# Kernel tuning notes

Hardware: AMD Instinct MI355X
Metric: run time of the kernel (lower is better)

The kernel has to match this reference:

```python
import jax, jax.numpy as jnp
import numpy as np

N = 100000
E = 1250000
D = 64
R = 16


def _glorot(key, shape):
    fan_in, fan_out = shape[-2], shape[-1]
    lim = jnp.sqrt(6.0 / (fan_in + fan_out))
    return jax.random.uniform(key, shape, jnp.float32, -lim, lim)


def setup_inputs() -> dict:
    key = jax.random.key(0)
    ks = jax.random.split(key, 9)
    x = jax.random.normal(ks[0], (N, D), jnp.float32)
    edge_index = jax.random.randint(ks[1], (2, E), 0, N, jnp.int64 if jax.config.jax_enable_x64 else jnp.int32).astype(jnp.int32)
    edge_type = jax.random.randint(ks[2], (E,), 0, R).astype(jnp.int32)
    return {
        "x": x,
        "edge_index": edge_index,
        "edge_type": edge_type,
        "W1": _glorot(ks[3], (R, D, D)),
        "sw1": _glorot(ks[4], (D, D)),
        "b1": jnp.zeros((D,), jnp.float32),
        "W2": _glorot(ks[5], (R, D, D)),
        "sw2": _glorot(ks[6], (D, D)),
        "b2": jnp.zeros((D,), jnp.float32),
    }


def _rgcn_layer(x, src, dst, edge_type, W, sw, b, residual):
    # self transform [N, O]
    out = x @ sw
    # per-relation transform of all nodes: [N, R, O] (avoids [E, D, O] gathered weights,
    # same math as bmm(x_j, W[edge_type]))
    xW = jnp.einsum('nd,rdo->nro', x, W)
    msg = xW[src, edge_type]                      # [E, O] per-edge messages
    agg = jax.ops.segment_sum(msg, dst, num_segments=N)  # scatter-add aggregate
    out = out + agg
    if residual:
        out = out + x  # Identity residual (in == out channels)
    out = out + b
    return jax.nn.relu(out)


def reference(x, edge_index, edge_type, W1, sw1, b1, W2, sw2, b2):
    src, dst = edge_index[0], edge_index[1]
    # layer 1: residual=True; layer 2: encoding=False -> no residual.
    # activation (relu) applied after every layer by RGCN.forward; dropout p=0 / eval -> no-op.
    h = _rgcn_layer(x, src, dst, edge_type, W1, sw1, b1, residual=True)
    h = _rgcn_layer(h, src, dst, edge_type, W2, sw2, b2, residual=False)
    return h
```

## Files before the change

### kernel.cpp

```cpp
#include <hip/hip_runtime.h>
#include <hip/hip_bf16.h>

#define NN 100000
#define NE 1250000
#define DD 64
#define RR 16
#define NP 17
#define NTILE 6250

typedef __attribute__((ext_vector_type(8))) short s16x8;
typedef __attribute__((ext_vector_type(4))) float f32x4;

static __device__ __forceinline__ unsigned short f2bf(float v) {
    __hip_bfloat16 h = __float2bfloat16(v);
    return __builtin_bit_cast(unsigned short, h);
}
static __device__ __forceinline__ float bf2f(unsigned short u) {
    unsigned int w = ((unsigned int)u) << 16;
    return __builtin_bit_cast(float, w);
}
static __device__ __forceinline__ unsigned int pack2(float a, float b) {
    return ((unsigned int)f2bf(b) << 16) | (unsigned int)f2bf(a);
}


__global__ void hist_dst(const int* __restrict__ dst, int* __restrict__ cnt) {
    int e = blockIdx.x * 256 + threadIdx.x;
    if (e < NE) atomicAdd(&cnt[dst[e]], 1);
}

__global__ __launch_bounds__(256) void scan1(const int* __restrict__ cnt,
                                             int* __restrict__ rp, int* __restrict__ part) {
    __shared__ int s[256];
    int i = blockIdx.x * 256 + threadIdx.x;
    int v = (i < NN) ? cnt[i] : 0;
    s[threadIdx.x] = v;
    __syncthreads();
    for (int off = 1; off < 256; off <<= 1) {
        int t = (threadIdx.x >= off) ? s[threadIdx.x - off] : 0;
        __syncthreads();
        s[threadIdx.x] += t;
        __syncthreads();
    }
    if (i < NN) rp[i] = s[threadIdx.x] - v;
    if (threadIdx.x == 255) part[blockIdx.x] = s[255];
}

#define NBLK_SCAN 391
__global__ void scan2(int* __restrict__ part, int* __restrict__ rp) {
    __shared__ int s[NBLK_SCAN];
    if (threadIdx.x < NBLK_SCAN) s[threadIdx.x] = part[threadIdx.x];
    __syncthreads();
    if (threadIdx.x == 0) {
        int acc = 0;
        for (int b = 0; b < NBLK_SCAN; ++b) { int t = s[b]; s[b] = acc; acc += t; }
        rp[NN] = NE;
    }
    __syncthreads();
    if (threadIdx.x < NBLK_SCAN) part[threadIdx.x] = s[threadIdx.x];
}

__global__ void scan3(int* __restrict__ rp, const int* __restrict__ part, int* __restrict__ cur) {
    int i = blockIdx.x * 256 + threadIdx.x;
    if (i < NN) {
        int v = rp[i] + part[blockIdx.x];
        rp[i] = v;
        cur[i] = v;
    }
}

__global__ void scatter_dst(const int* __restrict__ src, const int* __restrict__ dst,
                            const int* __restrict__ et, int* __restrict__ cur,
                            int* __restrict__ sg) {
    int e = blockIdx.x * 256 + threadIdx.x;
    if (e >= NE) return;
    int p = atomicAdd(&cur[dst[e]], 1);
    sg[p] = et[e] * NN + src[e];
}


__global__ void prep_w2(const float* __restrict__ W1, const float* __restrict__ sw1,
                        const float* __restrict__ W2, const float* __restrict__ sw2,
                        unsigned short* __restrict__ wt) {
    int i = blockIdx.x * 256 + threadIdx.x;
    if (i >= 2 * NP * DD * DD) return;
    int d = i & 63;
    int o = (i >> 6) & 63;
    int p = (i >> 12) % NP;
    int l = i / (NP * DD * DD);
    const float* src;
    if (p < 16) src = (l ? W2 : W1) + p * DD * DD;
    else        src = (l ? sw2 : sw1);
    wt[i] = f2bf(src[d * DD + o]);
}

__global__ void prep_x2(const float* __restrict__ x, unsigned short* __restrict__ xb) {
    int i = blockIdx.x * blockDim.x + threadIdx.x;
    if (i < NN * DD) xb[i] = f2bf(x[i]);
}

__global__ __launch_bounds__(256) void xw_kernel(
    const unsigned short* __restrict__ xb,
    const unsigned short* __restrict__ wt,
    unsigned short* __restrict__ tab)
{
    const int wid  = threadIdx.x >> 6;
    const int lane = threadIdx.x & 63;
    const int c = lane & 15;
    const int q = lane >> 4;
    const int t = blockIdx.x * 4 + wid;
    if (t >= NTILE) return;
    const int n0 = t * 16;
    const int p0 = blockIdx.y * 4;
    const int p1 = min(p0 + 4, NP);

    const unsigned short* xrow = xb + (size_t)(n0 + c) * DD + q * 8;
    s16x8 b0 = *(const s16x8*)(xrow);
    s16x8 b1 = *(const s16x8*)(xrow + 32);

    for (int p = p0; p < p1; ++p) {
        const unsigned short* wp = wt + p * (DD * DD);
        uint2* orow = (uint2*)(tab + ((size_t)p * NN + n0 + c) * DD);
        #pragma unroll
        for (int nb = 0; nb < 4; ++nb) {
            const unsigned short* wrow = wp + (nb * 16 + c) * DD + q * 8;
            s16x8 a0 = *(const s16x8*)(wrow);
            s16x8 a1 = *(const s16x8*)(wrow + 32);
            f32x4 acc = {0.f, 0.f, 0.f, 0.f};
            acc = __builtin_amdgcn_mfma_f32_16x16x32_bf16(a0, b0, acc, 0, 0, 0);
            acc = __builtin_amdgcn_mfma_f32_16x16x32_bf16(a1, b1, acc, 0, 0, 0);
            uint2 pk;
            pk.x = pack2(acc[0], acc[1]);
            pk.y = pack2(acc[2], acc[3]);
            orow[nb * 4 + q] = pk;
        }
    }
}

__global__ __launch_bounds__(256) void agg_kernel(
    const unsigned short* __restrict__ tab,
    const int* __restrict__ rp,
    const int* __restrict__ sg,
    const float* __restrict__ bias,
    const float* __restrict__ xres,
    float* __restrict__ outf,
    unsigned short* __restrict__ outb)
{
    const int wid  = threadIdx.x >> 6;
    const int lane = threadIdx.x & 63;
    const int n = blockIdx.x * 4 + wid;
    const int h  = lane >> 5;
    const int ol = lane & 31;

    float a0 = 0.f, a1 = 0.f;
    int e = rp[n];
    const int e1 = rp[n + 1];
    for (; e + 4 <= e1; e += 4) {
        int r0 = sg[e + h];
        int r1 = sg[e + 2 + h];
        unsigned int u0 = *(const unsigned int*)(tab + (size_t)r0 * DD + ol * 2);
        unsigned int u1 = *(const unsigned int*)(tab + (size_t)r1 * DD + ol * 2);
        a0 += bf2f((unsigned short)u0) + bf2f((unsigned short)u1);
        a1 += bf2f((unsigned short)(u0 >> 16)) + bf2f((unsigned short)(u1 >> 16));
    }
    for (; e + 2 <= e1; e += 2) {
        int r0 = sg[e + h];
        unsigned int u0 = *(const unsigned int*)(tab + (size_t)r0 * DD + ol * 2);
        a0 += bf2f((unsigned short)u0);
        a1 += bf2f((unsigned short)(u0 >> 16));
    }
    if (e < e1 && h == 0) {
        int r0 = sg[e];
        unsigned int u0 = *(const unsigned int*)(tab + (size_t)r0 * DD + ol * 2);
        a0 += bf2f((unsigned short)u0);
        a1 += bf2f((unsigned short)(u0 >> 16));
    }
    a0 += __shfl_xor(a0, 32, 64);
    a1 += __shfl_xor(a1, 32, 64);

    {
        unsigned int u = *(const unsigned int*)(tab + ((size_t)16 * NN + n) * DD + ol * 2);
        a0 += bf2f((unsigned short)u);
        a1 += bf2f((unsigned short)(u >> 16));
    }
    const float2 bv = *(const float2*)(bias + ol * 2);
    a0 += bv.x; a1 += bv.y;
    if (xres) {
        const float2 rv = *(const float2*)(xres + (size_t)n * DD + ol * 2);
        a0 += rv.x; a1 += rv.y;
    }
    a0 = fmaxf(a0, 0.f);
    a1 = fmaxf(a1, 0.f);

    if (h == 0) {
        if (outb)
            *(unsigned int*)(outb + (size_t)n * DD + ol * 2) = pack2(a0, a1);
        if (outf) {
            float2 v = {a0, a1};
            *(float2*)(outf + (size_t)n * DD + ol * 2) = v;
        }
    }
}


extern "C" void kernel_launch(void* const* d_in, const int* in_sizes, int n_in,
                              void* d_out, int out_size, void* d_ws, size_t ws_size,
                              hipStream_t stream)
{
    (void)in_sizes; (void)n_in; (void)out_size; (void)ws_size;
    const float* x    = (const float*)d_in[0];
    const int*   ei   = (const int*)d_in[1];
    const int*   et   = (const int*)d_in[2];
    const float* W1   = (const float*)d_in[3];
    const float* sw1  = (const float*)d_in[4];
    const float* b1   = (const float*)d_in[5];
    const float* W2   = (const float*)d_in[6];
    const float* sw2  = (const float*)d_in[7];
    const float* b2   = (const float*)d_in[8];
    float* out = (float*)d_out;

    const int* src = ei;
    const int* dst = ei + NE;

    char* ws = (char*)d_ws;

    unsigned short* tab  = (unsigned short*)(ws);
    unsigned short* xb   = (unsigned short*)(ws + 217600000);
    unsigned short* h1b  = (unsigned short*)(ws + 230400000);
    unsigned short* wt2  = (unsigned short*)(ws + 243200000);
    int* sg   = (int*)(ws + 243478528);
    int* rp   = (int*)(ws + 248478528);
    int* cur  = (int*)(ws + 248878544);
    int* cnt  = (int*)(ws + 249278544);
    int* part = (int*)(ws + 249678544);

    const int NB_E    = (NE + 255) / 256;
    const int NB_ELEM = (NN * DD + 255) / 256;

    hipMemsetAsync(cnt, 0, NN * sizeof(int), stream);
    hist_dst<<<NB_E, 256, 0, stream>>>(dst, cnt);
    scan1<<<NBLK_SCAN, 256, 0, stream>>>(cnt, rp, part);
    scan2<<<1, 512, 0, stream>>>(part, rp);
    scan3<<<NBLK_SCAN, 256, 0, stream>>>(rp, part, cur);
    scatter_dst<<<NB_E, 256, 0, stream>>>(src, dst, et, cur, sg);

    prep_w2<<<(2 * NP * DD * DD + 255) / 256, 256, 0, stream>>>(W1, sw1, W2, sw2, wt2);
    prep_x2<<<NB_ELEM, 256, 0, stream>>>(x, xb);

    const int NB_XW  = (NTILE + 3) / 4;
    const int NB_AGG = NN / 4;

    xw_kernel<<<dim3(NB_XW, 5), 256, 0, stream>>>(xb, wt2, tab);
    agg_kernel<<<NB_AGG, 256, 0, stream>>>(tab, rp, sg, b1, x, nullptr, h1b);

    xw_kernel<<<dim3(NB_XW, 5), 256, 0, stream>>>(h1b, wt2 + NP * DD * DD, tab);
    agg_kernel<<<NB_AGG, 256, 0, stream>>>(tab, rp, sg, b2, nullptr, out, nullptr);
}
```

Baseline: 598.2 us.

## Stage xW tile stores through LDS and give each agg node a half-wave

The xW kernel now writes each 16x64 bf16 output tile into padded LDS first, then copies it to global memory with contiguous coalesced 8-byte stores instead of scattered row-fragment stores. The aggregation kernel now gives each node a 32-lane half-wave instead of a full wave split into two halves. Each lane gathers four edges per iteration with no cross-half shuffle reduction, and the self term, bias and residual are loaded up front. This aims to raise store coalescing and memory-level parallelism in the gather, at the cost of extra LDS traffic and a more divergent edge tail.

New measurement: 535.5 us. -10.5%, faster.

```diff
diff --git a/kernel.cpp b/kernel.cpp
--- a/kernel.cpp
+++ b/kernel.cpp
@@ -7,6 +7,8 @@
 #define RR 16
 #define NP 17
 #define NTILE 6250
+#define NBLK_SCAN 391
+#define LST 68
 
 typedef __attribute__((ext_vector_type(8))) short s16x8;
 typedef __attribute__((ext_vector_type(4))) float f32x4;
@@ -46,7 +48,6 @@
     if (threadIdx.x == 255) part[blockIdx.x] = s[255];
 }
 
-#define NBLK_SCAN 391
 __global__ void scan2(int* __restrict__ part, int* __restrict__ rp) {
     __shared__ int s[NBLK_SCAN];
     if (threadIdx.x < NBLK_SCAN) s[threadIdx.x] = part[threadIdx.x];
@@ -88,10 +89,10 @@
     int o = (i >> 6) & 63;
     int p = (i >> 12) % NP;
     int l = i / (NP * DD * DD);
-    const float* src;
-    if (p < 16) src = (l ? W2 : W1) + p * DD * DD;
-    else        src = (l ? sw2 : sw1);
-    wt[i] = f2bf(src[d * DD + o]);
+    const float* srcp;
+    if (p < 16) srcp = (l ? W2 : W1) + p * DD * DD;
+    else        srcp = (l ? sw2 : sw1);
+    wt[i] = f2bf(srcp[d * DD + o]);
 }
 
 __global__ void prep_x2(const float* __restrict__ x, unsigned short* __restrict__ xb) {
@@ -104,6 +105,7 @@
     const unsigned short* __restrict__ wt,
     unsigned short* __restrict__ tab)
 {
+    __shared__ unsigned short lds[4][16 * LST];
     const int wid  = threadIdx.x >> 6;
     const int lane = threadIdx.x & 63;
     const int c = lane & 15;
@@ -118,9 +120,10 @@
     s16x8 b0 = *(const s16x8*)(xrow);
     s16x8 b1 = *(const s16x8*)(xrow + 32);
 
+    unsigned short* lw = lds[wid];
+
     for (int p = p0; p < p1; ++p) {
         const unsigned short* wp = wt + p * (DD * DD);
-        uint2* orow = (uint2*)(tab + ((size_t)p * NN + n0 + c) * DD);
         #pragma unroll
         for (int nb = 0; nb < 4; ++nb) {
             const unsigned short* wrow = wp + (nb * 16 + c) * DD + q * 8;
@@ -132,7 +135,16 @@
             uint2 pk;
             pk.x = pack2(acc[0], acc[1]);
             pk.y = pack2(acc[2], acc[3]);
-            orow[nb * 4 + q] = pk;
+            *(uint2*)&lw[c * LST + nb * 16 + q * 4] = pk;
+        }
+        unsigned short* gbase = tab + ((size_t)p * NN + n0) * DD;
+        #pragma unroll
+        for (int j = 0; j < 4; ++j) {
+            int i8 = lane + 64 * j;
+            int node = i8 >> 4;
+            int k8 = i8 & 15;
+            uint2 v = *(const uint2*)&lw[node * LST + k8 * 4];
+            *(uint2*)(gbase + (size_t)i8 * 4) = v;
         }
     }
 }
@@ -143,62 +155,62 @@
     const int* __restrict__ sg,
     const float* __restrict__ bias,
     const float* __restrict__ xres,
-    float* __restrict__ outf,
-    unsigned short* __restrict__ outb)
+    unsigned short* __restrict__ outb,
+    float* __restrict__ outf)
 {
-    const int wid  = threadIdx.x >> 6;
-    const int lane = threadIdx.x & 63;
-    const int n = blockIdx.x * 4 + wid;
-    const int h  = lane >> 5;
-    const int ol = lane & 31;
-
-    float a0 = 0.f, a1 = 0.f;
+    const int hw = threadIdx.x >> 5;
+    const int ll = threadIdx.x & 31;
+    const int n = blockIdx.x * 8 + hw;
+    const unsigned int* t32 = (const unsigned int*)tab;
+
+    unsigned int us = t32[((size_t)16 * NN + n) * 32 + ll];
+    const float2 bv = *(const float2*)(bias + ll * 2);
+    float a0 = bv.x + bf2f((unsigned short)us);
+    float a1 = bv.y + bf2f((unsigned short)(us >> 16));
+    if (xres) {
+        const float2 rv = *(const float2*)(xres + (size_t)n * DD + ll * 2);
+        a0 += rv.x; a1 += rv.y;
+    }
+
     int e = rp[n];
     const int e1 = rp[n + 1];
     for (; e + 4 <= e1; e += 4) {
-        int r0 = sg[e + h];
-        int r1 = sg[e + 2 + h];
-        unsigned int u0 = *(const unsigned int*)(tab + (size_t)r0 * DD + ol * 2);
-        unsigned int u1 = *(const unsigned int*)(tab + (size_t)r1 * DD + ol * 2);
+        int r0 = sg[e], r1 = sg[e + 1], r2 = sg[e + 2], r3 = sg[e + 3];
+        unsigned int u0 = t32[(size_t)r0 * 32 + ll];
+        unsigned int u1 = t32[(size_t)r1 * 32 + ll];
+        unsigned int u2 = t32[(size_t)r2 * 32 + ll];
+        unsigned int u3 = t32[(size_t)r3 * 32 + ll];
         a0 += bf2f((unsigned short)u0) + bf2f((unsigned short)u1);
         a1 += bf2f((unsigned short)(u0 >> 16)) + bf2f((unsigned short)(u1 >> 16));
-    }
-    for (; e + 2 <= e1; e += 2) {
-        int r0 = sg[e + h];
-        unsigned int u0 = *(const unsigned int*)(tab + (size_t)r0 * DD + ol * 2);
-        a0 += bf2f((unsigned short)u0);
-        a1 += bf2f((unsigned short)(u0 >> 16));
-    }
-    if (e < e1 && h == 0) {
-        int r0 = sg[e];
-        unsigned int u0 = *(const unsigned int*)(tab + (size_t)r0 * DD + ol * 2);
-        a0 += bf2f((unsigned short)u0);
-        a1 += bf2f((unsigned short)(u0 >> 16));
-    }
-    a0 += __shfl_xor(a0, 32, 64);
-    a1 += __shfl_xor(a1, 32, 64);
-
+        a0 += bf2f((unsigned short)u2) + bf2f((unsigned short)u3);
+        a1 += bf2f((unsigned short)(u2 >> 16)) + bf2f((unsigned short)(u3 >> 16));
+    }
     {
-        unsigned int u = *(const unsigned int*)(tab + ((size_t)16 * NN + n) * DD + ol * 2);
-        a0 += bf2f((unsigned short)u);
-        a1 += bf2f((unsigned short)(u >> 16));
-    }
-    const float2 bv = *(const float2*)(bias + ol * 2);
-    a0 += bv.x; a1 += bv.y;
-    if (xres) {
-        const float2 rv = *(const float2*)(xres + (size_t)n * DD + ol * 2);
-        a0 += rv.x; a1 += rv.y;
-    }
+        const int m = e1 - e;
+        int rA = (m > 0) ? sg[e]     : -1;
+        int rB = (m > 1) ? sg[e + 1] : -1;
+        int rC = (m > 2) ? sg[e + 2] : -1;
+        if (rA >= 0) {
+            unsigned int u = t32[(size_t)rA * 32 + ll];
+            a0 += bf2f((unsigned short)u); a1 += bf2f((unsigned short)(u >> 16));
+        }
+        if (rB >= 0) {
+            unsigned int u = t32[(size_t)rB * 32 + ll];
+            a0 += bf2f((unsigned short)u); a1 += bf2f((unsigned short)(u >> 16));
+        }
+        if (rC >= 0) {
+            unsigned int u = t32[(size_t)rC * 32 + ll];
+            a0 += bf2f((unsigned short)u); a1 += bf2f((unsigned short)(u >> 16));
+        }
+    }
+
     a0 = fmaxf(a0, 0.f);
     a1 = fmaxf(a1, 0.f);
-
-    if (h == 0) {
-        if (outb)
-            *(unsigned int*)(outb + (size_t)n * DD + ol * 2) = pack2(a0, a1);
-        if (outf) {
-            float2 v = {a0, a1};
-            *(float2*)(outf + (size_t)n * DD + ol * 2) = v;
-        }
+    if (outb)
+        *(unsigned int*)(outb + (size_t)n * DD + ll * 2) = pack2(a0, a1);
+    if (outf) {
+        float2 v = {a0, a1};
+        *(float2*)(outf + (size_t)n * DD + ll * 2) = v;
     }
 }
 
@@ -219,11 +231,10 @@
     const float* b2   = (const float*)d_in[8];
     float* out = (float*)d_out;
 
-    const int* src = ei;
-    const int* dst = ei + NE;
+    const int* srcA = ei;
+    const int* dstA = ei + NE;
 
     char* ws = (char*)d_ws;
-
     unsigned short* tab  = (unsigned short*)(ws);
     unsigned short* xb   = (unsigned short*)(ws + 217600000);
     unsigned short* h1b  = (unsigned short*)(ws + 230400000);
@@ -238,21 +249,22 @@
     const int NB_ELEM = (NN * DD + 255) / 256;
 
     hipMemsetAsync(cnt, 0, NN * sizeof(int), stream);
-    hist_dst<<<NB_E, 256, 0, stream>>>(dst, cnt);
+    hist_dst<<<NB_E, 256, 0, stream>>>(dstA, cnt);
     scan1<<<NBLK_SCAN, 256, 0, stream>>>(cnt, rp, part);
     scan2<<<1, 512, 0, stream>>>(part, rp);
     scan3<<<NBLK_SCAN, 256, 0, stream>>>(rp, part, cur);
-    scatter_dst<<<NB_E, 256, 0, stream>>>(src, dst, et, cur, sg);
+    scatter_dst<<<NB_E, 256, 0, stream>>>(srcA, dstA, et, cur, sg);
 
     prep_w2<<<(2 * NP * DD * DD + 255) / 256, 256, 0, stream>>>(W1, sw1, W2, sw2, wt2);
     prep_x2<<<NB_ELEM, 256, 0, stream>>>(x, xb);
 
     const int NB_XW  = (NTILE + 3) / 4;
-    const int NB_AGG = NN / 4;
+    const int NB_AGG = NN / 8;
+    const int WPL = NP * DD * DD;
 
     xw_kernel<<<dim3(NB_XW, 5), 256, 0, stream>>>(xb, wt2, tab);
-    agg_kernel<<<NB_AGG, 256, 0, stream>>>(tab, rp, sg, b1, x, nullptr, h1b);
-
-    xw_kernel<<<dim3(NB_XW, 5), 256, 0, stream>>>(h1b, wt2 + NP * DD * DD, tab);
-    agg_kernel<<<NB_AGG, 256, 0, stream>>>(tab, rp, sg, b2, nullptr, out, nullptr);
-}
+    agg_kernel<<<NB_AGG, 256, 0, stream>>>(tab, rp, sg, b1, x, h1b, nullptr);
+
+    xw_kernel<<<dim3(NB_XW, 5), 256, 0, stream>>>(h1b, wt2 + WPL, tab);
+    agg_kernel<<<NB_AGG, 256, 0, stream>>>(tab, rp, sg, b2, nullptr, nullptr, out);
+}
```
